# Kernel optimization log

Hardware: AMD Instinct MI355X
Metric: run time of the kernel (lower is better)

Reference implementation:

```python
import jax, jax.numpy as jnp
import numpy as np

N = 262144          # nodes
E = N * 16          # edges (avg degree 16)
C_IN = 64
C_OUT = 64
GRID = 0.5          # voxel size
POS_EXTENT = 10.0   # pos in [0, 10)^3
NVOX_DIM = int(round(POS_EXTENT / GRID))  # 20
NVOX = NVOX_DIM ** 3                      # 8000 voxels
BN_EPS = 1e-5


def setup_inputs() -> dict:
    key = jax.random.key(0)
    k = jax.random.split(key, 5)
    x = jax.random.normal(k[0], (N, C_IN), dtype=jnp.float32)
    pos = jax.random.uniform(k[1], (N, 3), dtype=jnp.float32, minval=0.0, maxval=POS_EXTENT)
    edge_index = jax.random.randint(k[2], (2, E), 0, N, dtype=jnp.int32)
    W = jax.random.normal(k[3], (C_IN, C_OUT), dtype=jnp.float32) / np.float32(np.sqrt(C_IN))
    b = jnp.zeros((C_OUT,), jnp.float32)
    gamma = jnp.ones((C_OUT,), jnp.float32)
    beta = jnp.zeros((C_OUT,), jnp.float32)
    return {"x": x, "pos": pos, "edge_index": edge_index,
            "W": W, "b": b, "gamma": gamma, "beta": beta}


def reference(x, pos, edge_index, W, b, gamma, beta):
    # --- self.down: Linear -> BatchNorm1d (training-mode batch stats) -> ReLU ---
    h = x @ W + b                                   # [N, C_OUT]
    mean = jnp.mean(h, axis=0)
    var = jnp.mean(jnp.square(h - mean), axis=0)    # biased variance (torch BN)
    h = (h - mean) * jax.lax.rsqrt(var + BN_EPS) * gamma + beta
    h = jax.nn.relu(h)

    # --- max_pool_neighbor_x: scatter-max of neighbor features (self-loops added) ---
    row, col = edge_index[0], edge_index[1]
    pooled = jax.ops.segment_max(h[row], col, num_segments=N)  # [N, C_OUT]
    h = jnp.maximum(pooled, h)  # self-loop; also fixes -inf for isolated nodes

    # --- GridSampling: voxel-grid quantize + per-voxel mean of x and pos ---
    vid = jnp.clip(jnp.floor(pos / GRID).astype(jnp.int32), 0, NVOX_DIM - 1)  # [N,3]
    vox = (vid[:, 0] * NVOX_DIM + vid[:, 1]) * NVOX_DIM + vid[:, 2]           # [N]
    cnt = jax.ops.segment_sum(jnp.ones((N,), jnp.float32), vox, num_segments=NVOX)
    x_sum = jax.ops.segment_sum(h, vox, num_segments=NVOX)     # [NVOX, C_OUT]
    p_sum = jax.ops.segment_sum(pos, vox, num_segments=NVOX)   # [NVOX, 3]
    denom = jnp.maximum(cnt, 1.0)[:, None]
    x_out = x_sum / denom
    pos_out = p_sum / denom
    # concat features and positions of the downsampled graph: [NVOX, C_OUT+3]
    return jnp.concatenate([x_out, pos_out], axis=1)
```

## Files before the change

kernel.cpp:

```cpp
#include <hip/hip_runtime.h>
#include <hip/hip_fp16.h>

#define NVOX_DIM 20
#define NVOX 8000
#define BN_EPS 1e-5f

#define NBUCK 1024
#define BSHIFT 8
#define NODES_PER_BUCK 256
#define GEMM_BLOCKS 1024
#define XTRA_BLOCKS 64
#define CAP_NEW 8192
#define CAP_OLD 5120
#define VCAP 88
#define CSTRIDE 16
#define VSTRIDE 4
#define BIN_EPB 16384

typedef _Float16 f16x8 __attribute__((ext_vector_type(8)));
typedef float f32x4 __attribute__((ext_vector_type(4)));

__device__ __forceinline__ unsigned short f2key(float v) {
    unsigned short hb = __half_as_ushort(__float2half(v));
    unsigned short m = (unsigned short)(0x8000u | (unsigned short)(-(int)(hb >> 15)));
    return (unsigned short)(hb ^ m);
}

__device__ __forceinline__ float key2f(unsigned int k) {
    unsigned short hb = (k & 0x8000u) ? (unsigned short)(k ^ 0x8000u)
                                      : (unsigned short)(0xFFFFu ^ k);
    __half_raw hr;
    hr.x = hb;
    return __half2float((__half)hr);
}

__device__ __forceinline__ f16x8 pack8(float4 a, float4 b) {
    f16x8 r;
    r[0] = (_Float16)a.x; r[1] = (_Float16)a.y; r[2] = (_Float16)a.z; r[3] = (_Float16)a.w;
    r[4] = (_Float16)b.x; r[5] = (_Float16)b.y; r[6] = (_Float16)b.z; r[7] = (_Float16)b.w;
    return r;
}

__device__ __forceinline__ void gemm_step(int row0, f16x8 a0, f16x8 a1,
                                          const f16x8 (&bf)[4][2], const float (&bv)[4],
                                          float (&s)[4], float (&s2)[4],
                                          unsigned short* __restrict__ h16,
                                          int l15, int q) {
#pragma unroll
    for (int t4 = 0; t4 < 4; ++t4) {
        f32x4 acc = {bv[t4], bv[t4], bv[t4], bv[t4]};
        acc = __builtin_amdgcn_mfma_f32_16x16x32_f16(a0, bf[t4][0], acc, 0, 0, 0);
        acc = __builtin_amdgcn_mfma_f32_16x16x32_f16(a1, bf[t4][1], acc, 0, 0, 0);
        s[t4] += acc[0] + acc[1] + acc[2] + acc[3];
        s2[t4] = fmaf(acc[0], acc[0], s2[t4]);
        s2[t4] = fmaf(acc[1], acc[1], s2[t4]);
        s2[t4] = fmaf(acc[2], acc[2], s2[t4]);
        s2[t4] = fmaf(acc[3], acc[3], s2[t4]);
#pragma unroll
        for (int r = 0; r < 4; ++r) {
            h16[(size_t)(row0 + q * 4 + r) * 64 + t4 * 16 + l15] = f2key(acc[r]);
        }
    }
}

__global__ __launch_bounds__(256) void k_zero(int* __restrict__ p, int n) {
    int i = blockIdx.x * 256 + threadIdx.x;
    if (i < n) p[i] = 0;
}

__global__ __launch_bounds__(256, 5) void k0_gemm(const float* __restrict__ x,
                                                  const float* __restrict__ W,
                                                  const float* __restrict__ bias,
                                                  unsigned short* __restrict__ h16,
                                                  float* __restrict__ partials, int n16,
                                                  const float* __restrict__ pos,
                                                  int* __restrict__ vcursor,
                                                  int* __restrict__ vlist) {
    __shared__ float sW[4096];
    __shared__ float red[2][4][64];
    int t = threadIdx.x;
    int bid = blockIdx.x;

    if (bid >= GEMM_BLOCKS) {
        int zb = bid - GEMM_BLOCKS;
        int nNodes = n16 * 16;
        for (int nd = zb * 256 + t; nd < nNodes; nd += XTRA_BLOCKS * 256) {
            float px = pos[(size_t)nd * 3 + 0];
            float py = pos[(size_t)nd * 3 + 1];
            float pz = pos[(size_t)nd * 3 + 2];
            int v0 = min(max((int)floorf(px * 2.f), 0), NVOX_DIM - 1);
            int v1 = min(max((int)floorf(py * 2.f), 0), NVOX_DIM - 1);
            int v2 = min(max((int)floorf(pz * 2.f), 0), NVOX_DIM - 1);
            int vox = (v0 * NVOX_DIM + v1) * NVOX_DIM + v2;
            int idx = atomicAdd(&vcursor[vox * VSTRIDE], 1);
            if (idx < VCAP) vlist[vox * VCAP + idx] = nd;
        }
        return;
    }

    int gb = bid;
    for (int i = t; i < 4096; i += 256) sW[i] = W[i];
    __syncthreads();
    int lane = t & 63;
    int w = t >> 6;
    int l15 = lane & 15;
    int q = lane >> 4;

    f16x8 bf[4][2];
#pragma unroll
    for (int t4 = 0; t4 < 4; ++t4)
#pragma unroll
        for (int kb = 0; kb < 2; ++kb)
#pragma unroll
            for (int i = 0; i < 8; ++i)
                bf[t4][kb][i] = (_Float16)sW[(kb * 32 + q * 8 + i) * 64 + t4 * 16 + l15];
    float bv[4];
#pragma unroll
    for (int t4 = 0; t4 < 4; ++t4) bv[t4] = bias[t4 * 16 + l15];

    float s[4] = {0.f, 0.f, 0.f, 0.f}, s2[4] = {0.f, 0.f, 0.f, 0.f};

#pragma unroll
    for (int kk = 0; kk < 2; ++kk) {
        int gA = gb * 4 + w + kk * (GEMM_BLOCKS * 8);
        int gB = gA + GEMM_BLOCKS * 4;
        bool doA = gA < n16, doB = gB < n16;
        float4 A0, A1, A2, A3, B0, B1, B2, B3;
        if (doA) {
            const float* xpA = x + (size_t)(gA * 16 + l15) * 64 + q * 8;
            A0 = *(const float4*)(xpA);
            A1 = *(const float4*)(xpA + 4);
            A2 = *(const float4*)(xpA + 32);
            A3 = *(const float4*)(xpA + 36);
        }
        if (doB) {
            const float* xpB = x + (size_t)(gB * 16 + l15) * 64 + q * 8;
            B0 = *(const float4*)(xpB);
            B1 = *(const float4*)(xpB + 4);
            B2 = *(const float4*)(xpB + 32);
            B3 = *(const float4*)(xpB + 36);
        }
        if (doA) {
            gemm_step(gA * 16, pack8(A0, A1), pack8(A2, A3), bf, bv, s, s2, h16, l15, q);
        }
        if (doB) {
            gemm_step(gB * 16, pack8(B0, B1), pack8(B2, B3), bf, bv, s, s2, h16, l15, q);
        }
    }

#pragma unroll
    for (int t4 = 0; t4 < 4; ++t4) {
        s[t4] += __shfl_xor(s[t4], 16, 64);
        s[t4] += __shfl_xor(s[t4], 32, 64);
        s2[t4] += __shfl_xor(s2[t4], 16, 64);
        s2[t4] += __shfl_xor(s2[t4], 32, 64);
    }
    if (lane < 16) {
#pragma unroll
        for (int t4 = 0; t4 < 4; ++t4) {
            red[0][w][t4 * 16 + lane] = s[t4];
            red[1][w][t4 * 16 + lane] = s2[t4];
        }
    }
    __syncthreads();
    if (t < 128) {
        int c = t & 63;
        int which = t >> 6;
        float v = red[which][0][c] + red[which][1][c] + red[which][2][c] + red[which][3][c];
        partials[(size_t)gb * 128 + which * 64 + c] = v;
    }
}

__global__ __launch_bounds__(1024) void k_bin2(const int* __restrict__ rows,
                                               const int* __restrict__ cols,
                                               int* __restrict__ cursor,
                                               unsigned int* __restrict__ pairs) {
    __shared__ unsigned int buf[BIN_EPB];
    __shared__ int hist[NBUCK];
    __shared__ int wpos[NBUCK];
    __shared__ int gbase[NBUCK];
    __shared__ int wsum[16];
    int t = threadIdx.x;
    int lane = t & 63;
    int w = t >> 6;

    hist[t] = 0;
    __syncthreads();

    int base_e = blockIdx.x * BIN_EPB + t * 16;
    int r[16], c[16];
#pragma unroll
    for (int g4 = 0; g4 < 4; ++g4) {
        int e = base_e + g4 * 4;
        int4 r4 = *(const int4*)(rows + e);
        int4 c4 = *(const int4*)(cols + e);
        r[g4 * 4 + 0] = r4.x; c[g4 * 4 + 0] = c4.x;
        r[g4 * 4 + 1] = r4.y; c[g4 * 4 + 1] = c4.y;
        r[g4 * 4 + 2] = r4.z; c[g4 * 4 + 2] = c4.z;
        r[g4 * 4 + 3] = r4.w; c[g4 * 4 + 3] = c4.w;
    }
#pragma unroll
    for (int i = 0; i < 16; ++i) atomicAdd(&hist[c[i] >> BSHIFT], 1);
    __syncthreads();

    int v = hist[t];
    int inc = v;
    for (int d = 1; d < 64; d <<= 1) {
        int u = __shfl_up(inc, d, 64);
        if (lane >= d) inc += u;
    }
    if (lane == 63) wsum[w] = inc;
    __syncthreads();
    int add = 0;
    for (int ww = 0; ww < w; ++ww) add += wsum[ww];
    wpos[t] = inc - v + add;
    gbase[t] = atomicAdd(&cursor[t * CSTRIDE], v);
    __syncthreads();

#pragma unroll
    for (int i = 0; i < 16; ++i) {
        int bkt = c[i] >> BSHIFT;
        int idx = atomicAdd(&wpos[bkt], 1);
        buf[idx] = ((unsigned int)r[i] << 8) | (unsigned int)(c[i] & (NODES_PER_BUCK - 1));
    }
    __syncthreads();

    for (int it = 0; it < 64; ++it) {
        int j = w * 64 + it;
        int cnt = hist[j];
        int src = wpos[j] - cnt;
        int dst0 = gbase[j];
        for (int k2 = lane; k2 < cnt; k2 += 64) {
            int d = dst0 + k2;
            if (d < CAP_NEW) pairs[(size_t)j * CAP_NEW + d] = buf[src + k2];
        }
    }
}

__global__ __launch_bounds__(1024) void k_pool_new(const unsigned int* __restrict__ pairs_,
                                                   const int* __restrict__ cursor,
                                                   const unsigned short* __restrict__ h16,
                                                   float* __restrict__ stats2,
                                                   unsigned short* __restrict__ pooled16,
                                                   const float* __restrict__ partials,
                                                   const float* __restrict__ gamma,
                                                   const float* __restrict__ beta,
                                                   float invN) {
    __shared__ unsigned int tile[NODES_PER_BUCK * 64];
    int b = blockIdx.x;
    int t = threadIdx.x;

    if (b == NBUCK) {
        float* fred = (float*)tile;
        float* tot = ((float*)tile) + 1024;
        int c = t & 127;
        int g = t >> 7;
        float s = 0.f;
        for (int pb = g; pb < GEMM_BLOCKS; pb += 8) s += partials[(size_t)pb * 128 + c];
        fred[g * 128 + c] = s;
        __syncthreads();
        if (t < 128) {
            float v = 0.f;
#pragma unroll
            for (int g2 = 0; g2 < 8; ++g2) v += fred[g2 * 128 + t];
            tot[t] = v;
        }
        __syncthreads();
        if (t < 64) {
            float mean = tot[t] * invN;
            float var = tot[64 + t] * invN - mean * mean;
            float sc = gamma[t] * rsqrtf(var + BN_EPS);
            stats2[t] = sc;
            stats2[64 + t] = beta[t] - mean * sc;
        }
        return;
    }

    int lane = t & 63;
    int w = t >> 6;

    const unsigned int* src = (const unsigned int*)(h16 + (size_t)b * (NODES_PER_BUCK * 64));
#pragma unroll
    for (int k = 0; k < 8; ++k) {
        int i = t + k * 1024;
        unsigned int u = src[i];
        tile[2 * i] = u & 0xFFFFu;
        tile[2 * i + 1] = u >> 16;
    }
    __syncthreads();

    int cntE = min(cursor[b * CSTRIDE], CAP_NEW);
    int start = b * CAP_NEW;
    int end = start + cntE;
    int chunk = (cntE + 15) >> 4;
    int cs = start + w * chunk;
    int ce = min(cs + chunk, end);
    for (int j0 = cs; j0 < ce; j0 += 64) {
        int lim = min(64, ce - j0);
        unsigned int pk = (lane < lim) ? pairs_[j0 + lane] : 0u;
        int jj = 0;
        for (; jj + 32 <= lim; jj += 32) {
            unsigned int qv[32];
            unsigned int vv[32];
#pragma unroll
            for (int u = 0; u < 32; ++u)
                qv[u] = (unsigned int)__builtin_amdgcn_readlane((int)pk, jj + u);
#pragma unroll
            for (int u = 0; u < 32; ++u)
                vv[u] = (unsigned int)h16[(size_t)(qv[u] >> 8) * 64 + lane];
#pragma unroll
            for (int u = 0; u < 32; ++u)
                atomicMax(&tile[((qv[u] & 255u) << 6) + lane], vv[u]);
        }
        for (; jj + 8 <= lim; jj += 8) {
            unsigned int qv[8];
            unsigned int vv[8];
#pragma unroll
            for (int u = 0; u < 8; ++u)
                qv[u] = (unsigned int)__builtin_amdgcn_readlane((int)pk, jj + u);
#pragma unroll
            for (int u = 0; u < 8; ++u)
                vv[u] = (unsigned int)h16[(size_t)(qv[u] >> 8) * 64 + lane];
#pragma unroll
            for (int u = 0; u < 8; ++u)
                atomicMax(&tile[((qv[u] & 255u) << 6) + lane], vv[u]);
        }
        for (; jj < lim; ++jj) {
            unsigned int qq = (unsigned int)__builtin_amdgcn_readlane((int)pk, jj);
            unsigned int v = h16[(size_t)(qq >> 8) * 64 + lane];
            atomicMax(&tile[((qq & 255u) << 6) + lane], v);
        }
    }
    __syncthreads();

#pragma unroll
    for (int nl = 0; nl < NODES_PER_BUCK; nl += 16) {
        int node_l = nl + w;
        pooled16[((size_t)((b << BSHIFT) + node_l)) * 64 + lane] =
            (unsigned short)tile[(node_l << 6) + lane];
    }
}

__global__ __launch_bounds__(256) void k_vox(const unsigned short* __restrict__ pooled16,
                                             const int* __restrict__ vlist,
                                             const int* __restrict__ vcursor,
                                             const float* __restrict__ pos,
                                             const float* __restrict__ stats2,
                                             float* __restrict__ out) {
    int v = blockIdx.x * 4 + (threadIdx.x >> 6);
    int lane = threadIdx.x & 63;
    int cv = vcursor[v * VSTRIDE];
    int c = min(cv, VCAP);
    float scale = stats2[lane], shift = stats2[64 + lane];
    const int* lst = vlist + (size_t)v * VCAP;
    float s0 = 0.f, s1 = 0.f, s2 = 0.f, s3 = 0.f;
    int i = 0;
    for (; i + 4 <= c; i += 4) {
        int n0 = lst[i], n1 = lst[i + 1], n2 = lst[i + 2], n3 = lst[i + 3];
        float v0 = key2f(pooled16[(size_t)n0 * 64 + lane]);
        float v1 = key2f(pooled16[(size_t)n1 * 64 + lane]);
        float v2 = key2f(pooled16[(size_t)n2 * 64 + lane]);
        float v3 = key2f(pooled16[(size_t)n3 * 64 + lane]);
        s0 += fmaxf(fmaf(v0, scale, shift), 0.f);
        s1 += fmaxf(fmaf(v1, scale, shift), 0.f);
        s2 += fmaxf(fmaf(v2, scale, shift), 0.f);
        s3 += fmaxf(fmaf(v3, scale, shift), 0.f);
    }
    for (; i < c; ++i) {
        float v0 = key2f(pooled16[(size_t)lst[i] * 64 + lane]);
        s0 += fmaxf(fmaf(v0, scale, shift), 0.f);
    }
    float den = 1.f / fmaxf((float)cv, 1.f);
    out[(size_t)v * 67 + lane] = (s0 + s1 + s2 + s3) * den;
    if (lane < 3) {
        float p0 = 0.f, p1 = 0.f, p2 = 0.f, p3 = 0.f;
        int j = 0;
        for (; j + 4 <= c; j += 4) {
            p0 += pos[(size_t)lst[j] * 3 + lane];
            p1 += pos[(size_t)lst[j + 1] * 3 + lane];
            p2 += pos[(size_t)lst[j + 2] * 3 + lane];
            p3 += pos[(size_t)lst[j + 3] * 3 + lane];
        }
        for (; j < c; ++j) p0 += pos[(size_t)lst[j] * 3 + lane];
        out[(size_t)v * 67 + 64 + lane] = (p0 + p1 + p2 + p3) * den;
    }
}

__global__ __launch_bounds__(256) void k0_fused_old(const float* __restrict__ x,
                                                    const float* __restrict__ W,
                                                    const float* __restrict__ bias,
                                                    unsigned short* __restrict__ h16,
                                                    float* __restrict__ partials, int n16,
                                                    const int* __restrict__ rows,
                                                    const int* __restrict__ cols,
                                                    int* __restrict__ cursor,
                                                    unsigned int* __restrict__ pairs,
                                                    float4* __restrict__ zero_zone,
                                                    int zero_n4) {
    __shared__ float sW[4096];
    __shared__ float red[2][4][64];
    __shared__ int lh[NBUCK];
    __shared__ int lpos[NBUCK];
    int t = threadIdx.x;
    int bid = blockIdx.x;

    if (bid >= 2 * GEMM_BLOCKS) {
        int zb = bid - 2 * GEMM_BLOCKS;
        float4 z = {0.f, 0.f, 0.f, 0.f};
        for (int i = zb * 256 + t; i < zero_n4; i += XTRA_BLOCKS * 256) zero_zone[i] = z;
        return;
    }

    if (bid & 1) {
        int bb = bid >> 1;
        for (int j = t; j < NBUCK; j += 256) lh[j] = 0;
        __syncthreads();
        int base = bb * 4096 + t * 16;
        int r[16], c[16];
#pragma unroll
        for (int g4 = 0; g4 < 4; ++g4) {
            int e = base + g4 * 4;
            int4 r4 = *(const int4*)(rows + e);
            int4 c4 = *(const int4*)(cols + e);
            r[g4 * 4 + 0] = r4.x; c[g4 * 4 + 0] = c4.x;
            r[g4 * 4 + 1] = r4.y; c[g4 * 4 + 1] = c4.y;
            r[g4 * 4 + 2] = r4.z; c[g4 * 4 + 2] = c4.z;
            r[g4 * 4 + 3] = r4.w; c[g4 * 4 + 3] = c4.w;
        }
#pragma unroll
        for (int i = 0; i < 16; ++i) atomicAdd(&lh[c[i] >> BSHIFT], 1);
        __syncthreads();
        for (int j = t; j < NBUCK; j += 256) lpos[j] = atomicAdd(&cursor[j], lh[j]);
        __syncthreads();
#pragma unroll
        for (int i = 0; i < 16; ++i) {
            int bkt = c[i] >> BSHIFT;
            int idx = atomicAdd(&lpos[bkt], 1);
            if (idx < CAP_OLD)
                pairs[(size_t)bkt * CAP_OLD + idx] =
                    ((unsigned int)r[i] << 8) | (unsigned int)(c[i] & (NODES_PER_BUCK - 1));
        }
        return;
    }

    int gb = bid >> 1;
    for (int i = t; i < 4096; i += 256) sW[i] = W[i];
    __syncthreads();
    int lane = t & 63;
    int w = t >> 6;
    int l15 = lane & 15;
    int q = lane >> 4;

    f16x8 bf[4][2];
#pragma unroll
    for (int t4 = 0; t4 < 4; ++t4)
#pragma unroll
        for (int kb = 0; kb < 2; ++kb)
#pragma unroll
            for (int i = 0; i < 8; ++i)
                bf[t4][kb][i] = (_Float16)sW[(kb * 32 + q * 8 + i) * 64 + t4 * 16 + l15];
    float bv[4];
#pragma unroll
    for (int t4 = 0; t4 < 4; ++t4) bv[t4] = bias[t4 * 16 + l15];

    float s[4] = {0.f, 0.f, 0.f, 0.f}, s2[4] = {0.f, 0.f, 0.f, 0.f};

    for (int g = gb * 4 + w; g < n16; g += GEMM_BLOCKS * 4) {
        int row0 = g * 16;
        const float* xp = x + (size_t)(row0 + l15) * 64 + q * 8;
        float4 xa = *(const float4*)(xp);
        float4 xb = *(const float4*)(xp + 4);
        float4 xc = *(const float4*)(xp + 32);
        float4 xd = *(const float4*)(xp + 36);
        gemm_step(row0, pack8(xa, xb), pack8(xc, xd), bf, bv, s, s2, h16, l15, q);
    }

#pragma unroll
    for (int t4 = 0; t4 < 4; ++t4) {
        s[t4] += __shfl_xor(s[t4], 16, 64);
        s[t4] += __shfl_xor(s[t4], 32, 64);
        s2[t4] += __shfl_xor(s2[t4], 16, 64);
        s2[t4] += __shfl_xor(s2[t4], 32, 64);
    }
    if (lane < 16) {
#pragma unroll
        for (int t4 = 0; t4 < 4; ++t4) {
            red[0][w][t4 * 16 + lane] = s[t4];
            red[1][w][t4 * 16 + lane] = s2[t4];
        }
    }
    __syncthreads();
    if (t < 128) {
        int c = t & 63;
        int which = t >> 6;
        float v = red[which][0][c] + red[which][1][c] + red[which][2][c] + red[which][3][c];
        partials[(size_t)gb * 128 + which * 64 + c] = v;
    }
}

__global__ __launch_bounds__(1024) void k3_finalize(const float* __restrict__ partials,
                                                    const float* __restrict__ gamma,
                                                    const float* __restrict__ beta,
                                                    float* __restrict__ stats2, float invN) {
    __shared__ float red[8][128];
    __shared__ float tot[128];
    int t = threadIdx.x;
    int c = t & 127;
    int g = t >> 7;
    float s = 0.f;
    for (int b = g; b < GEMM_BLOCKS; b += 8) s += partials[(size_t)b * 128 + c];
    red[g][c] = s;
    __syncthreads();
    if (t < 128) {
        float v = 0.f;
#pragma unroll
        for (int g2 = 0; g2 < 8; ++g2) v += red[g2][t];
        tot[t] = v;
    }
    __syncthreads();
    if (t < 64) {
        float mean = tot[t] * invN;
        float var = tot[64 + t] * invN - mean * mean;
        float sc = gamma[t] * rsqrtf(var + BN_EPS);
        stats2[t] = sc;
        stats2[64 + t] = beta[t] - mean * sc;
    }
}

__global__ __launch_bounds__(1024) void k_pool_old(const unsigned int* __restrict__ pairs_,
                                                   const int* __restrict__ cursor,
                                                   const unsigned short* __restrict__ h16,
                                                   const float* __restrict__ pos,
                                                   const float* __restrict__ stats2,
                                                   float* __restrict__ xs,
                                                   float* __restrict__ ps,
                                                   float* __restrict__ cnt) {
    __shared__ unsigned int tile[NODES_PER_BUCK * 64];
    int b = blockIdx.x;
    int t = threadIdx.x;
    int lane = t & 63;
    int w = t >> 6;
    float scale = stats2[lane];
    float shift = stats2[64 + lane];

    const unsigned int* src = (const unsigned int*)(h16 + (size_t)b * (NODES_PER_BUCK * 64));
#pragma unroll
    for (int k = 0; k < 8; ++k) {
        int i = t + k * 1024;
        unsigned int u = src[i];
        tile[2 * i] = u & 0xFFFFu;
        tile[2 * i + 1] = u >> 16;
    }
    __syncthreads();

    int cntE = min(cursor[b], CAP_OLD);
    int start = b * CAP_OLD;
    int end = start + cntE;
    int chunk = (cntE + 15) >> 4;
    int cs = start + w * chunk;
    int ce = min(cs + chunk, end);
    for (int j0 = cs; j0 < ce; j0 += 64) {
        int lim = min(64, ce - j0);
        unsigned int pk = (lane < lim) ? pairs_[j0 + lane] : 0u;
        int jj = 0;
        for (; jj + 16 <= lim; jj += 16) {
            unsigned int qv[16];
            unsigned short vv[16];
#pragma unroll
            for (int u = 0; u < 16; ++u)
                qv[u] = (unsigned int)__builtin_amdgcn_readlane((int)pk, jj + u);
#pragma unroll
            for (int u = 0; u < 16; ++u) vv[u] = h16[(size_t)(qv[u] >> 8) * 64 + lane];
#pragma unroll
            for (int u = 0; u < 16; ++u)
                atomicMax(&tile[((qv[u] & 255u) << 6) + lane], (unsigned int)vv[u]);
        }
        for (; jj < lim; ++jj) {
            unsigned int qq = (unsigned int)__builtin_amdgcn_readlane((int)pk, jj);
            unsigned int v = h16[(size_t)(qq >> 8) * 64 + lane];
            atomicMax(&tile[((qq & 255u) << 6) + lane], v);
        }
    }
    __syncthreads();

#pragma unroll
    for (int nl = 0; nl < NODES_PER_BUCK; nl += 16) {
        int node_l = nl + w;
        int c = (b << BSHIFT) + node_l;
        float px = pos[(size_t)c * 3 + 0];
        float py = pos[(size_t)c * 3 + 1];
        float pz = pos[(size_t)c * 3 + 2];
        int v0 = min(max((int)floorf(px * 2.f), 0), NVOX_DIM - 1);
        int v1 = min(max((int)floorf(py * 2.f), 0), NVOX_DIM - 1);
        int v2 = min(max((int)floorf(pz * 2.f), 0), NVOX_DIM - 1);
        int vox = (v0 * NVOX_DIM + v1) * NVOX_DIM + v2;
        float v = key2f(tile[(node_l << 6) + lane]);
        float val = fmaxf(fmaf(v, scale, shift), 0.f);
        atomicAdd(&xs[(size_t)vox * 64 + lane], val);
        if (lane < 3) atomicAdd(&ps[vox * 3 + lane], lane == 0 ? px : (lane == 1 ? py : pz));
        if (lane == 0) atomicAdd(&cnt[vox], 1.f);
    }
}

__global__ __launch_bounds__(256) void k7_out(const float* __restrict__ xs,
                                              const float* __restrict__ ps,
                                              const float* __restrict__ cnt,
                                              float* __restrict__ out, int total) {
    int idx = blockIdx.x * blockDim.x + threadIdx.x;
    if (idx >= total) return;
    int v = idx / 67;
    int c = idx - v * 67;
    float d = fmaxf(cnt[v], 1.f);
    float val = (c < 64) ? xs[(size_t)v * 64 + c] : ps[v * 3 + (c - 64)];
    out[idx] = val / d;
}

extern "C" void kernel_launch(void* const* d_in, const int* in_sizes, int n_in,
                              void* d_out, int out_size, void* d_ws, size_t ws_size,
                              hipStream_t stream) {
    const float* x     = (const float*)d_in[0];
    const float* pos   = (const float*)d_in[1];
    const int*   ei    = (const int*)d_in[2];
    const float* W     = (const float*)d_in[3];
    const float* b     = (const float*)d_in[4];
    const float* gamma = (const float*)d_in[5];
    const float* beta  = (const float*)d_in[6];
    float* out = (float*)d_out;

    const int n = in_sizes[0] / 64;
    const int E = in_sizes[2] / 2;
    char* ws = (char*)d_ws;

    const size_t NEED_NEW = 70643712;
    if (ws_size >= NEED_NEW) {
        unsigned short* h16      = (unsigned short*)(ws + 0);
        unsigned int*   pairs    = (unsigned int*)(ws + 33554432);
        unsigned short* pooled16 = (unsigned short*)(ws + 33554432);
        float*          partials = (float*)(ws + 67108864);
        float*          stats2   = (float*)(ws + 67633152);
        int*            cursor   = (int*)(ws + 67634176);
        int*            vcursor  = (int*)(ws + 67699712);
        int*            vlist    = (int*)(ws + 67827712);

        k_zero<<<189, 256, 0, stream>>>(cursor, 48384);
        k0_gemm<<<GEMM_BLOCKS + XTRA_BLOCKS, 256, 0, stream>>>(
            x, W, b, h16, partials, n >> 4, pos, vcursor, vlist);
        k_bin2<<<E / BIN_EPB, 1024, 0, stream>>>(ei, ei + E, cursor, pairs);
        k_pool_new<<<NBUCK + 1, 1024, 0, stream>>>(pairs, cursor, h16, stats2, pooled16,
                                                   partials, gamma, beta, 1.0f / (float)n);
        k_vox<<<NVOX / 4, 256, 0, stream>>>(pooled16, vlist, vcursor, pos, stats2, out);
    } else {
        unsigned short* h16      = (unsigned short*)(ws + 0);
        unsigned int*   pairs    = (unsigned int*)(ws + 33554432);
        float*          partials = (float*)(ws + 54525952);
        float*          stats2   = (float*)(ws + 55050240);
        int*            cursor   = (int*)(ws + 55051264);
        float*          xs       = (float*)(ws + 55055360);
        float*          ps       = (float*)(ws + 57103360);
        float*          cnt      = (float*)(ws + 57199360);
        float4*         zero4    = (float4*)(ws + 55055360);
        const int zero_n4 = (57231360 - 55055360) / 16;

        k_zero<<<4, 256, 0, stream>>>(cursor, NBUCK);
        k0_fused_old<<<2 * GEMM_BLOCKS + XTRA_BLOCKS, 256, 0, stream>>>(
            x, W, b, h16, partials, n >> 4, ei, ei + E, cursor, pairs, zero4, zero_n4);
        k3_finalize<<<1, 1024, 0, stream>>>(partials, gamma, beta, stats2, 1.0f / (float)n);
        k_pool_old<<<NBUCK, 1024, 0, stream>>>(pairs, cursor, h16, pos, stats2, xs, ps, cnt);
        k7_out<<<(out_size + 255) / 256, 256, 0, stream>>>(xs, ps, cnt, out, out_size);
    }
}
```

Baseline: 346.7 us.

## Stage GEMM output through LDS for coalesced h16 stores and widen blocks

The GEMM kernel now runs 512 threads (8 waves) per block, with each wave looping over 16-row tiles. Each tile's f16 keys are written to a padded LDS staging buffer and then stored to global memory as full contiguous 128-byte rows. Before, each lane scattered 2-byte stores across 16 separate rows. The aim is fewer, better-coalesced global writes, at the cost of extra LDS traffic and the loss of the explicit two-tile load prefetching the old loop had.

Result: faster. 311.5 us (-10.2%).

```diff
diff --git a/kernel.cpp b/kernel.cpp
--- a/kernel.cpp
+++ b/kernel.cpp
@@ -68,23 +68,24 @@
     if (i < n) p[i] = 0;
 }
 
-__global__ __launch_bounds__(256, 5) void k0_gemm(const float* __restrict__ x,
-                                                  const float* __restrict__ W,
-                                                  const float* __restrict__ bias,
-                                                  unsigned short* __restrict__ h16,
-                                                  float* __restrict__ partials, int n16,
-                                                  const float* __restrict__ pos,
-                                                  int* __restrict__ vcursor,
-                                                  int* __restrict__ vlist) {
+__global__ __launch_bounds__(512) void k0_gemm(const float* __restrict__ x,
+                                               const float* __restrict__ W,
+                                               const float* __restrict__ bias,
+                                               unsigned short* __restrict__ h16,
+                                               float* __restrict__ partials, int n16,
+                                               const float* __restrict__ pos,
+                                               int* __restrict__ vcursor,
+                                               int* __restrict__ vlist) {
     __shared__ float sW[4096];
-    __shared__ float red[2][4][64];
+    __shared__ float red[2][8][64];
+    __shared__ unsigned short stg[8][16][65];
     int t = threadIdx.x;
     int bid = blockIdx.x;
 
     if (bid >= GEMM_BLOCKS) {
         int zb = bid - GEMM_BLOCKS;
         int nNodes = n16 * 16;
-        for (int nd = zb * 256 + t; nd < nNodes; nd += XTRA_BLOCKS * 256) {
+        for (int nd = zb * 512 + t; nd < nNodes; nd += XTRA_BLOCKS * 512) {
             float px = pos[(size_t)nd * 3 + 0];
             float py = pos[(size_t)nd * 3 + 1];
             float pz = pos[(size_t)nd * 3 + 2];
@@ -99,7 +100,7 @@
     }
 
     int gb = bid;
-    for (int i = t; i < 4096; i += 256) sW[i] = W[i];
+    for (int i = t; i < 4096; i += 512) sW[i] = W[i];
     __syncthreads();
     int lane = t & 63;
     int w = t >> 6;
@@ -120,32 +121,32 @@
 
     float s[4] = {0.f, 0.f, 0.f, 0.f}, s2[4] = {0.f, 0.f, 0.f, 0.f};
 
-#pragma unroll
-    for (int kk = 0; kk < 2; ++kk) {
-        int gA = gb * 4 + w + kk * (GEMM_BLOCKS * 8);
-        int gB = gA + GEMM_BLOCKS * 4;
-        bool doA = gA < n16, doB = gB < n16;
-        float4 A0, A1, A2, A3, B0, B1, B2, B3;
-        if (doA) {
-            const float* xpA = x + (size_t)(gA * 16 + l15) * 64 + q * 8;
-            A0 = *(const float4*)(xpA);
-            A1 = *(const float4*)(xpA + 4);
-            A2 = *(const float4*)(xpA + 32);
-            A3 = *(const float4*)(xpA + 36);
-        }
-        if (doB) {
-            const float* xpB = x + (size_t)(gB * 16 + l15) * 64 + q * 8;
-            B0 = *(const float4*)(xpB);
-            B1 = *(const float4*)(xpB + 4);
-            B2 = *(const float4*)(xpB + 32);
-            B3 = *(const float4*)(xpB + 36);
-        }
-        if (doA) {
-            gemm_step(gA * 16, pack8(A0, A1), pack8(A2, A3), bf, bv, s, s2, h16, l15, q);
-        }
-        if (doB) {
-            gemm_step(gB * 16, pack8(B0, B1), pack8(B2, B3), bf, bv, s, s2, h16, l15, q);
-        }
+    for (int g = gb * 8 + w; g < n16; g += GEMM_BLOCKS * 8) {
+        int row0 = g * 16;
+        const float* xp = x + (size_t)(row0 + l15) * 64 + q * 8;
+        float4 xa = *(const float4*)(xp);
+        float4 xb = *(const float4*)(xp + 4);
+        float4 xc = *(const float4*)(xp + 32);
+        float4 xd = *(const float4*)(xp + 36);
+        f16x8 a0 = pack8(xa, xb), a1 = pack8(xc, xd);
+
+#pragma unroll
+        for (int t4 = 0; t4 < 4; ++t4) {
+            f32x4 acc = {bv[t4], bv[t4], bv[t4], bv[t4]};
+            acc = __builtin_amdgcn_mfma_f32_16x16x32_f16(a0, bf[t4][0], acc, 0, 0, 0);
+            acc = __builtin_amdgcn_mfma_f32_16x16x32_f16(a1, bf[t4][1], acc, 0, 0, 0);
+            s[t4] += acc[0] + acc[1] + acc[2] + acc[3];
+            s2[t4] = fmaf(acc[0], acc[0], s2[t4]);
+            s2[t4] = fmaf(acc[1], acc[1], s2[t4]);
+            s2[t4] = fmaf(acc[2], acc[2], s2[t4]);
+            s2[t4] = fmaf(acc[3], acc[3], s2[t4]);
+#pragma unroll
+            for (int r = 0; r < 4; ++r)
+                stg[w][q * 4 + r][t4 * 16 + l15] = f2key(acc[r]);
+        }
+#pragma unroll
+        for (int i = 0; i < 16; ++i)
+            h16[(size_t)(row0 + i) * 64 + lane] = stg[w][i][lane];
     }
 
 #pragma unroll
@@ -166,7 +167,9 @@
     if (t < 128) {
         int c = t & 63;
         int which = t >> 6;
-        float v = red[which][0][c] + red[which][1][c] + red[which][2][c] + red[which][3][c];
+        float v = 0.f;
+#pragma unroll
+        for (int ww = 0; ww < 8; ++ww) v += red[which][ww][c];
         partials[(size_t)gb * 128 + which * 64 + c] = v;
     }
 }
@@ -643,7 +646,7 @@
         int*            vlist    = (int*)(ws + 67827712);
 
         k_zero<<<189, 256, 0, stream>>>(cursor, 48384);
-        k0_gemm<<<GEMM_BLOCKS + XTRA_BLOCKS, 256, 0, stream>>>(
+        k0_gemm<<<GEMM_BLOCKS + XTRA_BLOCKS, 512, 0, stream>>>(
             x, W, b, h16, partials, n >> 4, pos, vcursor, vlist);
         k_bin2<<<E / BIN_EPB, 1024, 0, stream>>>(ei, ei + E, cursor, pairs);
         k_pool_new<<<NBUCK + 1, 1024, 0, stream>>>(pairs, cursor, h16, stats2, pooled16,
```
